# Optimization experiments

Measured on AMD Instinct MI355X. Metric: run time of the kernel, lower is better.

The kernel has to match this reference:

```python
import jax, jax.numpy as jnp
import numpy as np

V, E, H, B, S, C = 50000, 300, 512, 128, 80, 6
HH = 2 * H  # hidden_dim * num_directions (BiDi=True)


def _gru_dir(x, w_ih, w_hh, b_ih, b_hh, reverse):
    # x: (b, t, e) -> (b, t, h); torch nn.GRU cell math
    Bv, T, _ = x.shape
    Hd = w_hh.shape[1]
    xg = jnp.einsum('bte,ge->btg', x, w_ih) + b_ih  # (b, t, 3h)
    if reverse:
        xg = xg[:, ::-1]
    def step(h, xt):
        gi_r, gi_z, gi_n = jnp.split(xt, 3, axis=-1)
        gh_r, gh_z, gh_n = jnp.split(h @ w_hh.T + b_hh, 3, axis=-1)
        r = jax.nn.sigmoid(gi_r + gh_r)
        z = jax.nn.sigmoid(gi_z + gh_z)
        n = jnp.tanh(gi_n + r * gh_n)
        hn = (1.0 - z) * n + z * h
        return hn, hn
    h0 = jnp.zeros((Bv, Hd), x.dtype)
    _, hs = jax.lax.scan(step, h0, jnp.swapaxes(xg, 0, 1))
    hs = jnp.swapaxes(hs, 0, 1)
    if reverse:
        hs = hs[:, ::-1]
    return hs


def _bigru(x, pf, pb):
    return jnp.concatenate([_gru_dir(x, *pf, reverse=False), _gru_dir(x, *pb, reverse=True)], axis=-1)


def _conv1d(x, w, b, d):
    y = jax.lax.conv_general_dilated(x, w, (1,), 'VALID', rhs_dilation=(d,),
                                     dimension_numbers=('NCH', 'OIH', 'NCH'))
    return y + b[None, :, None]


def _bn(x, g, b, m, v):
    # eval-mode BatchNorm1d with running stats
    return (x - m[None, :, None]) * (g[None, :, None] / jnp.sqrt(v[None, :, None] + 1e-5)) + b[None, :, None]


def setup_inputs():
    key = jax.random.key(0)
    ks = iter(jax.random.split(key, 64))
    def W(*shape):
        return jax.random.normal(next(ks), shape, jnp.float32) * 0.02
    inp = {
        'input_batch': jax.random.randint(next(ks), (B, S), 1, V),
        'choices_batch': jax.random.randint(next(ks), (B, 4, C), 1, V),
        'emb_table': W(V, E),
    }
    for p in ('sg', 'cg'):
        for d in ('f', 'b'):
            inp[p + '_wih_' + d] = W(3 * H, E)
            inp[p + '_whh_' + d] = W(3 * H, H)
            inp[p + '_bih_' + d] = W(3 * H)
            inp[p + '_bhh_' + d] = W(3 * H)
    inp['lin_w'] = W(HH, HH * C)
    inp['lin_b'] = W(HH)
    inp['attn_w'] = W(HH, HH)
    inp['attn_b'] = W(HH)
    inp['c11_w'] = W(HH, S, 3);  inp['c11_b'] = W(HH)
    inp['c13_w'] = W(HH, HH, 3); inp['c13_b'] = W(HH)
    inp['c21_w'] = W(HH, HH, 3); inp['c21_b'] = W(HH)
    inp['c23_w'] = W(HH, HH, 3); inp['c23_b'] = W(HH)
    for i in ('1', '2'):
        inp['bn' + i + '_g'] = jnp.ones((HH,), jnp.float32)
        inp['bn' + i + '_b'] = jnp.zeros((HH,), jnp.float32)
        inp['bn' + i + '_m'] = jnp.zeros((HH,), jnp.float32)
        inp['bn' + i + '_v'] = jnp.ones((HH,), jnp.float32)
    inp['gate_wp'] = W(2 * HH, HH)
    inp['gate_wc'] = W(2 * HH, 2 * HH)
    inp['gate_b'] = W(2 * HH)
    inp['out_wp'] = W(2 * HH, HH)
    inp['out_b'] = W(2 * HH)
    return inp


def reference(input_batch, choices_batch, emb_table,
              sg_wih_f, sg_whh_f, sg_bih_f, sg_bhh_f, sg_wih_b, sg_whh_b, sg_bih_b, sg_bhh_b,
              cg_wih_f, cg_whh_f, cg_bih_f, cg_bhh_f, cg_wih_b, cg_whh_b, cg_bih_b, cg_bhh_b,
              lin_w, lin_b, attn_w, attn_b,
              c11_w, c11_b, c13_w, c13_b, c21_w, c21_b, c23_w, c23_b,
              bn1_g, bn1_b, bn1_m, bn1_v, bn2_g, bn2_b, bn2_m, bn2_v,
              gate_wp, gate_wc, gate_b, out_wp, out_b):
    # --- encode passage: embedding + BiGRU (dropout is eval-mode identity) ---
    sent = _bigru(emb_table[input_batch],
                  (sg_wih_f, sg_whh_f, sg_bih_f, sg_bhh_f),
                  (sg_wih_b, sg_whh_b, sg_bih_b, sg_bhh_b))  # (B, S, 2h)
    cgf = (cg_wih_f, cg_whh_f, cg_bih_f, cg_bhh_f)
    cgb = (cg_wih_b, cg_whh_b, cg_bih_b, cg_bhh_b)

    def choice_vec(tok):  # (B, C) -> (B, 2h)
        g = _bigru(emb_table[tok], cgf, cgb)               # (B, C, 2h)
        return g.reshape(g.shape[0], -1) @ lin_w.T + lin_b

    cvs = [choice_vec(choices_batch[:, i]) for i in range(4)]

    # --- AttnReader: shared Wh/bh, per-choice softmax attention over seq ---
    Wh = jnp.einsum('bsh,hg->bsg', sent, attn_w)  # (B, S, 2h)
    bh = sent @ attn_b                            # (B, S)

    def attn_read(cv):
        a = jax.nn.softmax(jnp.einsum('bsg,bg->bs', Wh, cv) + bh, axis=1)
        return jnp.einsum('bs,bsh->bh', a, sent)  # (B, 2h)

    pars = [attn_read(cv) for cv in cvs]

    # --- IDCNN: Conv1d treats seq dim S as channels (faithful to source) ---
    x = jax.nn.relu(_bn(_conv1d(sent, c11_w, c11_b, 1), bn1_g, bn1_b, bn1_m, bn1_v))
    x = _conv1d(x, c13_w, c13_b, 3)
    x = jax.nn.relu(_bn(_conv1d(x, c21_w, c21_b, 1), bn2_g, bn2_b, bn2_m, bn2_v))
    x = _conv1d(x, c23_w, c23_b, 3)
    P = jnp.max(x, axis=2)  # AdaptiveMaxPool1d(1) + squeeze -> (B, 2h)

    Cs = [jnp.concatenate([cv, par], axis=1) for cv, par in zip(cvs, pars)]  # (B, 4h)

    # --- PointerNet (note: source bug makes out1..out4 all equal C1WP+bC1) ---
    WP = P @ gate_wp.T          # (B, 4h)
    WP_out = P @ out_wp.T       # (B, 4h)
    Cd1 = Cs[0] * jax.nn.sigmoid(WP + Cs[0] @ gate_wc.T + gate_b)
    o1 = jnp.sum(Cd1 * WP_out, axis=1, keepdims=True) + (Cd1 @ out_b)[:, None]  # (B, 1)
    return jnp.concatenate([o1, o1, o1, o1], axis=1)  # (B, 4)
```

## Files before the change

### kernel.cpp

```cpp
#include <hip/hip_runtime.h>

typedef unsigned int u32;
typedef unsigned short u16;
typedef __attribute__((ext_vector_type(4))) float f32x4;
typedef __attribute__((ext_vector_type(8))) short bf16x8;

#define DEV static __device__ __forceinline__

DEV float sigf(float x){ return 1.0f/(1.0f + expf(-x)); }

DEV u16 f2bf(float x){
  u32 u = __float_as_uint(x);
  u32 r = (u + 0x7FFFu + ((u >> 16) & 1u)) >> 16;
  return (u16)r;
}

DEV u32 encf(float f){
  u32 u = __float_as_uint(f);
  return (u & 0x80000000u) ? ~u : (u | 0x80000000u);
}
DEV float decf(u32 e){
  return (e & 0x80000000u) ? __uint_as_float(e ^ 0x80000000u) : __uint_as_float(~e);
}

DEV void gload16(const void* g, void* l){
  __builtin_amdgcn_global_load_lds((const __attribute__((address_space(1))) u32*)g,
                                   (__attribute__((address_space(3))) u32*)l, 16, 0, 0);
}

__global__ __launch_bounds__(256,2) void gemm_bf16(
    const u16* __restrict__ A, const u16* __restrict__ A2,
    const u16* __restrict__ B,
    const float* __restrict__ bias, const float* __restrict__ bias2,
    float* __restrict__ C, float* __restrict__ C2, int ldc,
    int Kp, int ksteps)
{
  __shared__ u16 lds[(128 + 128)*32];
  char* ldsc = (char*)&lds[0];
  const int Boff = 128*64;
  const int tid = threadIdx.x;
  const int l = tid & 63, w = tid >> 6;
  const int n0 = blockIdx.x * 128, m0 = blockIdx.y * 128;
  const u16* Ause = blockIdx.z ? A2 : A;
  const float* buse = blockIdx.z ? bias2 : bias;
  float* Cuse = blockIdx.z ? C2 : C;
  const int wr = w >> 1, wc = w & 1;
  const int lr = l & 15, g = l >> 4;

  f32x4 acc[4][4];
  #pragma unroll
  for (int i=0;i<4;++i)
    #pragma unroll
    for (int j=0;j<4;++j) acc[i][j] = f32x4{0.f,0.f,0.f,0.f};

  for (int ks = 0; ks < ksteps; ++ks) {
    const int i0 = ks*32;
    __syncthreads();
    #pragma unroll
    for (int r = 0; r < 2; ++r) {
      const int rr = w*2 + r;
      const int c = rr*64 + l;
      const int row = c >> 2, bpos = c & 3;
      const int ib = bpos ^ ((row>>1) & 3);
      gload16(Ause + ((size_t)(m0 + row)*Kp + (i0 + ib*8)), ldsc + rr*1024);
      gload16(B    + ((size_t)(n0 + row)*Kp + (i0 + ib*8)), ldsc + Boff + rr*1024);
    }
    __syncthreads();
    bf16x8 af[4], bfr[4];
    #pragma unroll
    for (int m=0;m<4;++m){
      int o = wr*64 + m*16 + lr;
      af[m] = *(const bf16x8*)(ldsc + o*64 + ((g ^ ((o>>1)&3))<<4));
    }
    #pragma unroll
    for (int n=0;n<4;++n){
      int pr = wc*64 + n*16 + lr;
      bfr[n] = *(const bf16x8*)(ldsc + Boff + pr*64 + ((g ^ ((pr>>1)&3))<<4));
    }
    #pragma unroll
    for (int m=0;m<4;++m)
      #pragma unroll
      for (int n=0;n<4;++n)
        acc[m][n] = __builtin_amdgcn_mfma_f32_16x16x32_bf16(af[m], bfr[n], acc[m][n], 0,0,0);
  }

  #pragma unroll
  for (int m=0;m<4;++m){
    int mm = m0 + wr*64 + m*16 + g*4;
    f32x4 bv = *(const f32x4*)(buse + mm);
    #pragma unroll
    for (int n=0;n<4;++n){
      int p = n0 + wc*64 + n*16 + lr;
      f32x4 v;
      #pragma unroll
      for (int r2=0;r2<4;++r2) v[r2] = acc[m][n][r2] + bv[r2];
      *(f32x4*)(Cuse + (size_t)p*ldc + mm) = v;
    }
  }
}

__global__ __launch_bounds__(256,2) void gemm_bf16_sk(
    const u16* __restrict__ A, const u16* __restrict__ B,
    float* __restrict__ C, int ldc, int Kp, int kpc)
{
  __shared__ u16 lds[(128 + 128)*32];
  char* ldsc = (char*)&lds[0];
  const int Boff = 128*64;
  const int tid = threadIdx.x;
  const int l = tid & 63, w = tid >> 6;
  const int n0 = blockIdx.x * 128, m0 = blockIdx.y * 128;
  const int ks0 = blockIdx.z * kpc;
  const int wr = w >> 1, wc = w & 1;
  const int lr = l & 15, g = l >> 4;

  f32x4 acc[4][4];
  #pragma unroll
  for (int i=0;i<4;++i)
    #pragma unroll
    for (int j=0;j<4;++j) acc[i][j] = f32x4{0.f,0.f,0.f,0.f};

  for (int ks = 0; ks < kpc; ++ks) {
    const int i0 = (ks0 + ks)*32;
    __syncthreads();
    #pragma unroll
    for (int r = 0; r < 2; ++r) {
      const int rr = w*2 + r;
      const int c = rr*64 + l;
      const int row = c >> 2, bpos = c & 3;
      const int ib = bpos ^ ((row>>1) & 3);
      gload16(A + ((size_t)(m0 + row)*Kp + (i0 + ib*8)), ldsc + rr*1024);
      gload16(B + ((size_t)(n0 + row)*Kp + (i0 + ib*8)), ldsc + Boff + rr*1024);
    }
    __syncthreads();
    bf16x8 af[4], bfr[4];
    #pragma unroll
    for (int m=0;m<4;++m){
      int o = wr*64 + m*16 + lr;
      af[m] = *(const bf16x8*)(ldsc + o*64 + ((g ^ ((o>>1)&3))<<4));
    }
    #pragma unroll
    for (int n=0;n<4;++n){
      int pr = wc*64 + n*16 + lr;
      bfr[n] = *(const bf16x8*)(ldsc + Boff + pr*64 + ((g ^ ((pr>>1)&3))<<4));
    }
    #pragma unroll
    for (int m=0;m<4;++m)
      #pragma unroll
      for (int n=0;n<4;++n)
        acc[m][n] = __builtin_amdgcn_mfma_f32_16x16x32_bf16(af[m], bfr[n], acc[m][n], 0,0,0);
  }

  #pragma unroll
  for (int m=0;m<4;++m){
    int mm = m0 + wr*64 + m*16 + g*4;
    #pragma unroll
    for (int n=0;n<4;++n){
      int p = n0 + wc*64 + n*16 + lr;
      float* dst = C + (size_t)p*ldc + mm;
      #pragma unroll
      for (int r2=0;r2<4;++r2) atomicAdd(dst + r2, acc[m][n][r2]);
    }
  }
}

__global__ void initc(float* __restrict__ C, const float* __restrict__ bias,
                      int total, int mmask)
{
  int i = blockIdx.x*256 + threadIdx.x;
  if (i < total) C[i] = bias ? bias[i & mmask] : 0.f;
}

__global__ __launch_bounds__(256) void gru_step(
    const float* __restrict__ xg0, const float* __restrict__ xg1,
    const float* __restrict__ whh0, const float* __restrict__ whh1,
    const float* __restrict__ bhh0, const float* __restrict__ bhh1,
    float* __restrict__ hs, int S, int t)
{
  __shared__ float hL[32*520];
  __shared__ float wL[48*132];
  const int tid = threadIdx.x;
  const int tj = tid & 15, tb = tid >> 4;
  const int jg = blockIdx.x;
  const int b0 = blockIdx.y*32;
  const int dir = blockIdx.z;
  const int l = tid & 63, w = tid >> 6;
  const float* xg  = dir ? xg1  : xg0;
  const float* whh = dir ? whh1 : whh0;
  const float* bhh = dir ? bhh1 : bhh0;
  const int tt = dir ? (S-1-t) : t;
  const int j = jg*16 + tj;

  float accr[2], accz[2], accn[2];
  {
    float br = bhh[j], bz = bhh[512+j], bn = bhh[1024+j];
    accr[0]=br; accr[1]=br; accz[0]=bz; accz[1]=bz; accn[0]=bn; accn[1]=bn;
  }

  if (t > 0){
    const int tp = dir ? (tt+1) : (tt-1);
    #pragma unroll
    for (int rr = 0; rr < 8; ++rr){
      int row = w*8 + rr;
      const float* srcb = hs + ((size_t)(b0+row)*S + tp)*1024 + dir*512;
      gload16(srcb + l*4,       (char*)hL + (size_t)(row*520)*4);
      gload16(srcb + 256 + l*4, (char*)hL + (size_t)(row*520 + 256)*4);
    }
    for (int c = 0; c < 4; ++c){
      const int k0 = c*128;
      __syncthreads();
      #pragma unroll
      for (int i = 0; i < 6; ++i){
        int qidx = tid + i*256;
        int row = qidx >> 5, q = qidx & 31;
        int grow = (row>>4)*512 + jg*16 + (row & 15);
        f32x4 v = *(const f32x4*)(whh + (size_t)grow*512 + k0 + q*4);
        *(f32x4*)(wL + row*132 + q*4) = v;
      }
      __syncthreads();
      #pragma unroll 4
      for (int q = 0; q < 32; ++q){
        f32x4 ha  = *(const f32x4*)(hL + (2*tb  )*520 + k0 + q*4);
        f32x4 hb  = *(const f32x4*)(hL + (2*tb+1)*520 + k0 + q*4);
        f32x4 wr4 = *(const f32x4*)(wL + tj*132      + q*4);
        f32x4 wz4 = *(const f32x4*)(wL + (16+tj)*132 + q*4);
        f32x4 wn4 = *(const f32x4*)(wL + (32+tj)*132 + q*4);
        #pragma unroll
        for (int e = 0; e < 4; ++e){
          accr[0] += ha[e]*wr4[e]; accz[0] += ha[e]*wz4[e]; accn[0] += ha[e]*wn4[e];
          accr[1] += hb[e]*wr4[e]; accz[1] += hb[e]*wz4[e]; accn[1] += hb[e]*wn4[e];
        }
      }
    }
  }

  #pragma unroll
  for (int bi = 0; bi < 2; ++bi){
    int lb = 2*tb + bi;
    int b = b0 + lb;
    size_t xbase = ((size_t)b*S + tt)*1536;
    float gir = xg[xbase + j], giz = xg[xbase + 512 + j], gin = xg[xbase + 1024 + j];
    float hp = (t>0) ? hL[lb*520 + j] : 0.f;
    float r = sigf(gir + accr[bi]);
    float z = sigf(giz + accz[bi]);
    float n = tanhf(gin + r*accn[bi]);
    hs[((size_t)b*S + tt)*1024 + dir*512 + j] = (1.f - z)*n + z*hp;
  }
}

__global__ void transpose_sent(const float* __restrict__ sent, u16* __restrict__ sentT)
{
  __shared__ float tl[80][65];
  int b = blockIdx.y, h0 = blockIdx.x*64;
  for (int idx = threadIdx.x; idx < 80*64; idx += 256){
    int s = idx >> 6, hh = idx & 63;
    tl[s][hh] = sent[((size_t)b*80 + s)*1024 + h0 + hh];
  }
  __syncthreads();
  for (int idx = threadIdx.x; idx < 64*96; idx += 256){
    int hh = idx / 96, s = idx % 96;
    sentT[((size_t)b*1024 + h0 + hh)*96 + s] = (s < 80) ? f2bf(tl[s][hh]) : (u16)0;
  }
}

__global__ void attn_scores(const float* __restrict__ sent, const float* __restrict__ u,
                            const float* __restrict__ attn_b, float* __restrict__ sc)
{
  int wid = blockIdx.x*4 + (threadIdx.x >> 6);
  int lane = threadIdx.x & 63;
  const float* row = sent + (size_t)wid*1024;
  const float* ub = u + (size_t)(wid/80)*1024;
  float acc = 0.f;
  for (int h = lane; h < 1024; h += 64) acc += row[h]*(ub[h] + attn_b[h]);
  #pragma unroll
  for (int m = 32; m; m >>= 1) acc += __shfl_xor(acc, m);
  if (lane == 0) sc[wid] = acc;
}

__global__ void softmax80(const float* __restrict__ sc, float* __restrict__ a)
{
  int b = blockIdx.x, l = threadIdx.x;
  float v0 = sc[b*80 + l];
  float v1 = (l < 16) ? sc[b*80 + 64 + l] : -1e30f;
  float mx = fmaxf(v0, v1);
  #pragma unroll
  for (int m = 32; m; m >>= 1) mx = fmaxf(mx, __shfl_xor(mx, m));
  float e0 = expf(v0 - mx);
  float e1 = (l < 16) ? expf(v1 - mx) : 0.f;
  float s = e0 + e1;
  #pragma unroll
  for (int m = 32; m; m >>= 1) s += __shfl_xor(s, m);
  float inv = 1.f/s;
  a[b*80 + l] = e0*inv;
  if (l < 16) a[b*80 + 64 + l] = e1*inv;
}

__global__ void par_cs0(const float* __restrict__ a, const float* __restrict__ sent,
                        const float* __restrict__ cv, float* __restrict__ Cs0)
{
  int b = blockIdx.x;
  for (int h = threadIdx.x; h < 1024; h += 256){
    float acc = 0.f;
    for (int s = 0; s < 80; ++s) acc += a[b*80+s]*sent[((size_t)b*80+s)*1024 + h];
    Cs0[(size_t)b*2048 + 1024 + h] = acc;
    Cs0[(size_t)b*2048 + h] = cv[(size_t)b*1024 + h];
  }
}

__global__ void pack_w(const float* __restrict__ src, u16* __restrict__ dst,
                       int O, int CIs, int CIp)
{
  int i = blockIdx.x*256 + threadIdx.x;
  int total = 3*O*CIp;
  if (i >= total) return;
  int tap = i/(O*CIp); int rem = i%(O*CIp); int o = rem/CIp, ci = rem%CIp;
  float v = (ci < CIs) ? src[((size_t)o*CIs + ci)*3 + tap] : 0.f;
  dst[((size_t)tap*O + o)*CIp + ci] = f2bf(v);
}

__global__ void pack_wk(const float* __restrict__ src, u16* __restrict__ dst,
                        int M, int Ks, int Kp)
{
  int i = blockIdx.x*256 + threadIdx.x;
  if (i >= M*Kp) return;
  int row = i/Kp, k = i%Kp;
  dst[i] = (k < Ks) ? f2bf(src[(size_t)row*Ks + k]) : (u16)0;
}

__global__ void pack_f2b(const float* __restrict__ src, u16* __restrict__ dst, int n)
{
  int i = blockIdx.x*256 + threadIdx.x;
  if (i < n) dst[i] = f2bf(src[i]);
}

__global__ void pack_x(const float* __restrict__ emb, const int* __restrict__ toks,
                       int rdiv, int rmul, u16* __restrict__ dst, int R)
{
  int i = blockIdx.x*256 + threadIdx.x;
  if (i >= R*320) return;
  int row = i/320, k = i%320;
  int tok = toks[(row/rdiv)*rmul + (row%rdiv)];
  dst[i] = (k < 300) ? f2bf(emb[(size_t)tok*300 + k]) : (u16)0;
}

__global__ void prep_ab(const float* c11b, const float* c13b, const float* c21b, const float* c23b,
                        const float* g1, const float* b1, const float* m1, const float* v1,
                        const float* g2, const float* b2, const float* m2, const float* v2,
                        float* ab)
{
  int i = blockIdx.x*256 + threadIdx.x;
  if (i >= 4096) return;
  int layer = i >> 10, o = i & 1023;
  float al, be;
  if (layer == 0){ al = g1[o]/sqrtf(v1[o]+1e-5f); be = c11b[o]*al + b1[o] - m1[o]*al; }
  else if (layer == 1){ al = 1.f; be = c13b[o]; }
  else if (layer == 2){ al = g2[o]/sqrtf(v2[o]+1e-5f); be = c21b[o]*al + b2[o] - m2[o]*al; }
  else { al = 1.f; be = c23b[o]; }
  ab[layer*2048 + o] = al;
  ab[layer*2048 + 1024 + o] = be;
}

__global__ void init_penc(u32* p){
  int i = blockIdx.x*256 + threadIdx.x;
  if (i < 128*1024) p[i] = encf(-3.3e38f);
}
__global__ void dec_p(const u32* __restrict__ pe, float* __restrict__ pf){
  int i = blockIdx.x*256 + threadIdx.x;
  if (i < 128*1024) pf[i] = decf(pe[i]);
}

__global__ __launch_bounds__(512,2) void conv_mfma(
    const u16* __restrict__ X, long bstrideX,
    const u16* __restrict__ Wt,
    const float* __restrict__ alpha, const float* __restrict__ beta,
    u16* __restrict__ Y, long bstrideY,
    u32* __restrict__ Penc, int b0,
    int P_in, int P_out, int CI, int dil, int ksteps, int mode)
{
  __shared__ u16 lds[2*66560/2];
  char* ldsc = (char*)&lds[0];
  const int BUF = 66560;
  const int BOFF = 768*64;
  const int tid = threadIdx.x;
  const int l = tid & 63, w = tid >> 6;
  const int wg = blockIdx.x + (blockIdx.y<<2) + (blockIdx.z<<4);
  const int id2 = ((wg & 7) << 5) | (wg >> 3);
  const int p0 = (id2 & 3) * 256;
  const int o0 = ((id2 >> 2) & 3) * 256;
  const int bz = id2 >> 4;
  const u16* Xb = X + (size_t)bz * (size_t)bstrideX;
  const int wr = w >> 2, wc = w & 3;
  const int lr = l & 15, g = l >> 4;

  f32x4 acc[8][4];
  #pragma unroll
  for (int i=0;i<8;++i)
    #pragma unroll
    for (int j=0;j<4;++j) acc[i][j] = f32x4{0.f,0.f,0.f,0.f};

  {
    const int i0 = 0;
    #pragma unroll
    for (int r = 0; r < 6; ++r) {
      const int c = r*512 + tid;
      const int row = c >> 2, bpos = c & 3;
      const int tap = row >> 8, o = row & 255;
      const int ib = bpos ^ ((row>>1) & 3);
      gload16(Wt + ((size_t)(tap*1024 + o0 + o)*CI + (i0 + ib*8)), ldsc + (size_t)c*16);
    }
    #pragma unroll
    for (int r = 0; r < 3; ++r) {
      const int c = r*512 + tid;
      if (c < 1088){
        const int row = c >> 2, bpos = c & 3;
        const int ib = bpos ^ ((row>>1) & 3);
        int ps = p0 + row; ps = ps < P_in ? ps : (P_in - 1);
        gload16(Xb + ((size_t)ps*CI + (i0 + ib*8)), ldsc + BOFF + (size_t)c*16);
      }
    }
  }
  __syncthreads();

  for (int ks = 0; ks < ksteps; ++ks) {
    const int cur = ks & 1;
    if (ks + 1 < ksteps) {
      const int i0 = (ks+1)*32;
      char* dst = ldsc + (cur^1)*BUF;
      #pragma unroll
      for (int r = 0; r < 6; ++r) {
        const int c = r*512 + tid;
        const int row = c >> 2, bpos = c & 3;
        const int tap = row >> 8, o = row & 255;
        const int ib = bpos ^ ((row>>1) & 3);
        gload16(Wt + ((size_t)(tap*1024 + o0 + o)*CI + (i0 + ib*8)), dst + (size_t)c*16);
      }
      #pragma unroll
      for (int r = 0; r < 3; ++r) {
        const int c = r*512 + tid;
        if (c < 1088){
          const int row = c >> 2, bpos = c & 3;
          const int ib = bpos ^ ((row>>1) & 3);
          int ps = p0 + row; ps = ps < P_in ? ps : (P_in - 1);
          gload16(Xb + ((size_t)ps*CI + (i0 + ib*8)), dst + BOFF + (size_t)c*16);
        }
      }
    }
    char* src = ldsc + cur*BUF;
    #pragma unroll
    for (int tap = 0; tap < 3; ++tap) {
      bf16x8 af[8];
      #pragma unroll
      for (int m=0;m<8;++m){
        int o = wr*128 + m*16 + lr;
        int row = tap*256 + o;
        af[m] = *(const bf16x8*)(src + row*64 + ((g ^ ((row>>1)&3))<<4));
      }
      #pragma unroll
      for (int n=0;n<4;++n){
        int pr = wc*64 + n*16 + lr + dil*tap;
        bf16x8 bfr = *(const bf16x8*)(src + BOFF + pr*64 + ((g ^ ((pr>>1)&3))<<4));
        #pragma unroll
        for (int m=0;m<8;++m)
          acc[m][n] = __builtin_amdgcn_mfma_f32_16x16x32_bf16(af[m], bfr, acc[m][n], 0,0,0);
      }
    }
    __syncthreads();
  }

  if (mode == 2) {
    #pragma unroll
    for (int m=0;m<8;++m){
      int oo = o0 + wr*128 + m*16 + g*4;
      f32x4 al = *(const f32x4*)(alpha + oo);
      f32x4 be = *(const f32x4*)(beta + oo);
      float vm[4] = {-1e30f,-1e30f,-1e30f,-1e30f};
      #pragma unroll
      for (int n=0;n<4;++n){
        int p = p0 + wc*64 + n*16 + lr;
        bool ok = p < P_out;
        #pragma unroll
        for (int r2=0;r2<4;++r2){
          float v = acc[m][n][r2]*al[r2] + be[r2];
          vm[r2] = ok ? fmaxf(vm[r2], v) : vm[r2];
        }
      }
      #pragma unroll
      for (int r2=0;r2<4;++r2){
        float v = vm[r2];
        #pragma unroll
        for (int mask=1; mask<16; mask<<=1) v = fmaxf(v, __shfl_xor(v, mask));
        if (lr == 0) atomicMax(&Penc[(size_t)(b0+bz)*1024 + oo + r2], encf(v));
      }
    }
  } else {
    #pragma unroll
    for (int m=0;m<8;++m){
      int oo = o0 + wr*128 + m*16 + g*4;
      f32x4 al = *(const f32x4*)(alpha + oo);
      f32x4 be = *(const f32x4*)(beta + oo);
      #pragma unroll
      for (int n=0;n<4;++n){
        int p = p0 + wc*64 + n*16 + lr;
        if (p < P_out){
          float v0 = acc[m][n][0]*al[0] + be[0];
          float v1 = acc[m][n][1]*al[1] + be[1];
          float v2 = acc[m][n][2]*al[2] + be[2];
          float v3 = acc[m][n][3]*al[3] + be[3];
          if (mode == 0){ v0=fmaxf(v0,0.f); v1=fmaxf(v1,0.f); v2=fmaxf(v2,0.f); v3=fmaxf(v3,0.f); }
          uint2 pk;
          pk.x = (u32)f2bf(v0) | ((u32)f2bf(v1) << 16);
          pk.y = (u32)f2bf(v2) | ((u32)f2bf(v3) << 16);
          *(uint2*)(Y + (size_t)bz*(size_t)bstrideY + (size_t)p*1024 + oo) = pk;
        }
      }
    }
  }
}

__global__ void head_final(const float* __restrict__ Cs0, const float* __restrict__ t1,
                           const float* __restrict__ t2, const float* __restrict__ outb,
                           float* __restrict__ dout)
{
  __shared__ float red[256];
  int b = blockIdx.x;
  float part = 0.f;
  for (int gg = threadIdx.x; gg < 2048; gg += 256){
    float cd = Cs0[(size_t)b*2048+gg] * sigf(t1[(size_t)b*2048+gg]);
    part += cd * (t2[(size_t)b*2048+gg] + outb[gg]);
  }
  red[threadIdx.x] = part;
  __syncthreads();
  for (int s = 128; s > 0; s >>= 1){
    if (threadIdx.x < s) red[threadIdx.x] += red[threadIdx.x + s];
    __syncthreads();
  }
  if (threadIdx.x < 4) dout[b*4 + threadIdx.x] = red[0];
}

extern "C" void kernel_launch(void* const* d_in, const int* in_sizes, int n_in,
                              void* d_out, int out_size, void* d_ws, size_t ws_size,
                              hipStream_t stream)
{
  (void)in_sizes; (void)n_in; (void)out_size; (void)ws_size;
  const int*   input_batch = (const int*)d_in[0];
  const int*   choices     = (const int*)d_in[1];
  const float* emb    = (const float*)d_in[2];
  const float* sgwihf = (const float*)d_in[3];
  const float* sgwhhf = (const float*)d_in[4];
  const float* sgbihf = (const float*)d_in[5];
  const float* sgbhhf = (const float*)d_in[6];
  const float* sgwihb = (const float*)d_in[7];
  const float* sgwhhb = (const float*)d_in[8];
  const float* sgbihb = (const float*)d_in[9];
  const float* sgbhhb = (const float*)d_in[10];
  const float* cgwihf = (const float*)d_in[11];
  const float* cgwhhf = (const float*)d_in[12];
  const float* cgbihf = (const float*)d_in[13];
  const float* cgbhhf = (const float*)d_in[14];
  const float* cgwihb = (const float*)d_in[15];
  const float* cgwhhb = (const float*)d_in[16];
  const float* cgbihb = (const float*)d_in[17];
  const float* cgbhhb = (const float*)d_in[18];
  const float* lin_w  = (const float*)d_in[19];
  const float* lin_b  = (const float*)d_in[20];
  const float* attn_w = (const float*)d_in[21];
  const float* attn_b = (const float*)d_in[22];
  const float* c11w = (const float*)d_in[23];
  const float* c11b = (const float*)d_in[24];
  const float* c13w = (const float*)d_in[25];
  const float* c13b = (const float*)d_in[26];
  const float* c21w = (const float*)d_in[27];
  const float* c21b = (const float*)d_in[28];
  const float* c23w = (const float*)d_in[29];
  const float* c23b = (const float*)d_in[30];
  const float* bn1g = (const float*)d_in[31];
  const float* bn1b = (const float*)d_in[32];
  const float* bn1m = (const float*)d_in[33];
  const float* bn1v = (const float*)d_in[34];
  const float* bn2g = (const float*)d_in[35];
  const float* bn2b = (const float*)d_in[36];
  const float* bn2m = (const float*)d_in[37];
  const float* bn2v = (const float*)d_in[38];
  const float* gatewp = (const float*)d_in[39];
  const float* gatewc = (const float*)d_in[40];
  const float* gateb  = (const float*)d_in[41];
  const float* outwp  = (const float*)d_in[42];
  const float* outb   = (const float*)d_in[43];
  float* dout = (float*)d_out;

  char* ws = (char*)d_ws; size_t off = 0;
  auto alc = [&](size_t n)->char*{ char* p = ws + off; off = (off + n + 255) & ~(size_t)255; return p; };
  float* xg_f  = (float*)alc((size_t)128*80*1536*4);
  float* xg_b  = (float*)alc((size_t)128*80*1536*4);
  float* xg_cf = (float*)alc((size_t)128*6*1536*4);
  float* xg_cb = (float*)alc((size_t)128*6*1536*4);
  float* gh    = (float*)alc((size_t)2*128*1536*4); (void)gh;
  float* sent  = (float*)alc((size_t)128*80*1024*4);
  float* g_c   = (float*)alc((size_t)128*6*1024*4);
  u16*   sentT = (u16*)alc((size_t)128*1024*96*2);
  float* cv    = (float*)alc((size_t)128*1024*4);
  float* uu    = (float*)alc((size_t)128*1024*4);
  float* scb   = (float*)alc((size_t)128*80*4);
  float* aw    = (float*)alc((size_t)128*80*4);
  float* Cs0   = (float*)alc((size_t)128*2048*4);
  u16* W1p = (u16*)alc((size_t)3*1024*96*2);
  u16* W2p = (u16*)alc((size_t)3*1024*1024*2);
  u16* W3p = (u16*)alc((size_t)3*1024*1024*2);
  u16* W4p = (u16*)alc((size_t)3*1024*1024*2);
  float* ab  = (float*)alc((size_t)4*2048*4);
  u32*  Penc = (u32*)alc((size_t)128*1024*4);
  float* Pf  = (float*)alc((size_t)128*1024*4);
  float* t1  = (float*)alc((size_t)128*2048*4);
  float* t2  = (float*)alc((size_t)128*2048*4);
  u16* xbf_s = (u16*)alc((size_t)10240*320*2);
  u16* xbf_c = (u16*)alc((size_t)768*320*2);
  u16* Wsf = (u16*)alc((size_t)1536*320*2);
  u16* Wsb = (u16*)alc((size_t)1536*320*2);
  u16* Wcf = (u16*)alc((size_t)1536*320*2);
  u16* Wcb = (u16*)alc((size_t)1536*320*2);

  char* R1 = (char*)xg_f;
  u16* linw_bf  = (u16*)(R1);
  u16* attnw_bf = (u16*)(R1 + 12582912);
  u16* gcbf     = (u16*)(R1 + 14680064);
  u16* cvbf     = (u16*)(R1 + 16252928);
  const int bc = 16;
  u16* Y0 = (u16*)(R1 + 16515072);
  u16* Y1 = Y0 + (size_t)bc*1024*1024;
  char* R2 = (char*)sent;
  u16* gwp_bf = (u16*)(R2);
  u16* gwc_bf = (u16*)(R2 + 4194304);
  u16* owp_bf = (u16*)(R2 + 12582912);
  u16* Pfbf   = (u16*)(R2 + 16777216);
  u16* Cs0bf  = (u16*)(R2 + 17039360);

  dim3 T(256), T5(512);

  pack_w<<<dim3((3*1024*96+255)/256), T, 0, stream>>>(c11w, W1p, 1024, 80, 96);
  pack_w<<<dim3((3*1024*1024+255)/256), T, 0, stream>>>(c13w, W2p, 1024, 1024, 1024);
  pack_w<<<dim3((3*1024*1024+255)/256), T, 0, stream>>>(c21w, W3p, 1024, 1024, 1024);
  pack_w<<<dim3((3*1024*1024+255)/256), T, 0, stream>>>(c23w, W4p, 1024, 1024, 1024);
  pack_wk<<<dim3((1536*320+255)/256), T, 0, stream>>>(sgwihf, Wsf, 1536, 300, 320);
  pack_wk<<<dim3((1536*320+255)/256), T, 0, stream>>>(sgwihb, Wsb, 1536, 300, 320);
  pack_wk<<<dim3((1536*320+255)/256), T, 0, stream>>>(cgwihf, Wcf, 1536, 300, 320);
  pack_wk<<<dim3((1536*320+255)/256), T, 0, stream>>>(cgwihb, Wcb, 1536, 300, 320);
  pack_x<<<dim3((10240*320+255)/256), T, 0, stream>>>(emb, input_batch, 80, 80, xbf_s, 10240);
  pack_x<<<dim3((768*320+255)/256), T, 0, stream>>>(emb, choices, 6, 24, xbf_c, 768);
  prep_ab<<<16, T, 0, stream>>>(c11b, c13b, c21b, c23b,
                                bn1g,bn1b,bn1m,bn1v, bn2g,bn2b,bn2m,bn2v, ab);
  init_penc<<<512, T, 0, stream>>>(Penc);

  gemm_bf16<<<dim3(80,12,2), T, 0, stream>>>(Wsf, Wsb, xbf_s, sgbihf, sgbihb,
                                             xg_f, xg_b, 1536, 320, 10);
  gemm_bf16<<<dim3(6,12,2), T, 0, stream>>>(Wcf, Wcb, xbf_c, cgbihf, cgbihb,
                                            xg_cf, xg_cb, 1536, 320, 10);

  for (int t = 0; t < 80; ++t)
    gru_step<<<dim3(32,4,2), T, 0, stream>>>(xg_f, xg_b, sgwhhf, sgwhhb,
                                             sgbhhf, sgbhhb, sent, 80, t);
  for (int t = 0; t < 6; ++t)
    gru_step<<<dim3(32,4,2), T, 0, stream>>>(xg_cf, xg_cb, cgwhhf, cgwhhb,
                                             cgbhhf, cgbhhb, g_c, 6, t);

  pack_wk<<<dim3((1024*6144+255)/256), T, 0, stream>>>(lin_w, linw_bf, 1024, 6144, 6144);
  pack_wk<<<dim3((1024*1024+255)/256), T, 0, stream>>>(attn_w, attnw_bf, 1024, 1024, 1024);
  pack_f2b<<<dim3((128*6144+255)/256), T, 0, stream>>>(g_c, gcbf, 128*6144);

  transpose_sent<<<dim3(16,128), T, 0, stream>>>(sent, sentT);

  initc<<<dim3((128*1024+255)/256), T, 0, stream>>>(cv, lin_b, 128*1024, 1023);
  gemm_bf16_sk<<<dim3(1,8,6), T, 0, stream>>>(linw_bf, gcbf, cv, 1024, 6144, 32);
  pack_f2b<<<dim3((128*1024+255)/256), T, 0, stream>>>(cv, cvbf, 128*1024);
  initc<<<dim3((128*1024+255)/256), T, 0, stream>>>(uu, nullptr, 128*1024, 1023);
  gemm_bf16_sk<<<dim3(1,8,2), T, 0, stream>>>(attnw_bf, cvbf, uu, 1024, 1024, 16);
  attn_scores<<<2560, T, 0, stream>>>(sent, uu, attn_b, scb);
  softmax80<<<128, dim3(64), 0, stream>>>(scb, aw);
  par_cs0<<<128, T, 0, stream>>>(aw, sent, cv, Cs0);

  pack_wk<<<dim3((2048*1024+255)/256), T, 0, stream>>>(gatewp, gwp_bf, 2048, 1024, 1024);
  pack_wk<<<dim3((2048*2048+255)/256), T, 0, stream>>>(gatewc, gwc_bf, 2048, 2048, 2048);
  pack_wk<<<dim3((2048*1024+255)/256), T, 0, stream>>>(outwp, owp_bf, 2048, 1024, 1024);
  pack_f2b<<<dim3((128*2048+255)/256), T, 0, stream>>>(Cs0, Cs0bf, 128*2048);

  for (int b0 = 0; b0 < 128; b0 += bc){
    conv_mfma<<<dim3(4,4,bc), T5, 0, stream>>>(sentT + (size_t)b0*1024*96, (long)1024*96,
        W1p, ab+0,    ab+1024, Y0, (long)1024*1024, nullptr, 0, 1024, 1022, 96,   1, 3,  0);
    conv_mfma<<<dim3(4,4,bc), T5, 0, stream>>>(Y0, (long)1024*1024,
        W2p, ab+2048, ab+3072, Y1, (long)1024*1024, nullptr, 0, 1022, 1016, 1024, 3, 32, 1);
    conv_mfma<<<dim3(4,4,bc), T5, 0, stream>>>(Y1, (long)1024*1024,
        W3p, ab+4096, ab+5120, Y0, (long)1024*1024, nullptr, 0, 1016, 1014, 1024, 1, 32, 0);
    conv_mfma<<<dim3(4,4,bc), T5, 0, stream>>>(Y0, (long)1024*1024,
        W4p, ab+6144, ab+7168, nullptr, 0, Penc, b0,          1014, 1008, 1024, 3, 32, 2);
  }
  dec_p<<<512, T, 0, stream>>>(Penc, Pf);
  pack_f2b<<<dim3((128*1024+255)/256), T, 0, stream>>>(Pf, Pfbf, 128*1024);

  initc<<<dim3((128*2048+255)/256), T, 0, stream>>>(t1, gateb, 128*2048, 2047);
  gemm_bf16_sk<<<dim3(1,16,2), T, 0, stream>>>(gwp_bf, Pfbf, t1, 2048, 1024, 16);
  gemm_bf16_sk<<<dim3(1,16,4), T, 0, stream>>>(gwc_bf, Cs0bf, t1, 2048, 2048, 16);
  initc<<<dim3((128*2048+255)/256), T, 0, stream>>>(t2, nullptr, 128*2048, 2047);
  gemm_bf16_sk<<<dim3(1,16,2), T, 0, stream>>>(owp_bf, Pfbf, t2, 2048, 1024, 16);
  head_final<<<128, T, 0, stream>>>(Cs0, t1, t2, outb, dout);
}
```

Measured before the change: 3.720 ms.

## Overlap conv prefetch loads with MFMA compute using per-wave vmcnt waits

```diff
diff --git a/kernel.cpp b/kernel.cpp
--- a/kernel.cpp
+++ b/kernel.cpp
@@ -368,6 +368,36 @@
   if (i < 128*1024) pf[i] = decf(pe[i]);
 }
 
+#define CONV_STAGE(DST, I0)                                                   \
+  {                                                                           \
+    _Pragma("unroll")                                                         \
+    for (int r = 0; r < 6; ++r) {                                             \
+      const int c = r*512 + tid;                                              \
+      const int row = c >> 2, bpos = c & 3;                                   \
+      const int tap = row >> 8, o = row & 255;                                \
+      const int ib = bpos ^ ((row>>1) & 3);                                   \
+      gload16(Wt + ((size_t)(tap*1024 + o0 + o)*CI + ((I0) + ib*8)),          \
+              (DST) + (size_t)c*16);                                          \
+    }                                                                         \
+    _Pragma("unroll")                                                         \
+    for (int r = 0; r < 2; ++r) {                                             \
+      const int c = w*136 + r*64 + l;                                         \
+      const int row = c >> 2, bpos = c & 3;                                   \
+      const int ib = bpos ^ ((row>>1) & 3);                                   \
+      int ps = p0 + row; ps = ps < P_in ? ps : (P_in - 1);                    \
+      gload16(Xb + ((size_t)ps*CI + ((I0) + ib*8)),                           \
+              (DST) + BOFF + (size_t)c*16);                                   \
+    }                                                                         \
+    if (l < 8) {                                                              \
+      const int c = w*136 + 128 + l;                                          \
+      const int row = c >> 2, bpos = c & 3;                                   \
+      const int ib = bpos ^ ((row>>1) & 3);                                   \
+      int ps = p0 + row; ps = ps < P_in ? ps : (P_in - 1);                    \
+      gload16(Xb + ((size_t)ps*CI + ((I0) + ib*8)),                           \
+              (DST) + BOFF + (size_t)c*16);                                   \
+    }                                                                         \
+  }
+
 __global__ __launch_bounds__(512,2) void conv_mfma(
     const u16* __restrict__ X, long bstrideX,
     const u16* __restrict__ Wt,
@@ -376,7 +406,7 @@
     u32* __restrict__ Penc, int b0,
     int P_in, int P_out, int CI, int dil, int ksteps, int mode)
 {
-  __shared__ u16 lds[2*66560/2];
+  __shared__ u16 lds[66560];
   char* ldsc = (char*)&lds[0];
   const int BUF = 66560;
   const int BOFF = 768*64;
@@ -397,54 +427,22 @@
     #pragma unroll
     for (int j=0;j<4;++j) acc[i][j] = f32x4{0.f,0.f,0.f,0.f};
 
-  {
-    const int i0 = 0;
-    #pragma unroll
-    for (int r = 0; r < 6; ++r) {
-      const int c = r*512 + tid;
-      const int row = c >> 2, bpos = c & 3;
-      const int tap = row >> 8, o = row & 255;
-      const int ib = bpos ^ ((row>>1) & 3);
-      gload16(Wt + ((size_t)(tap*1024 + o0 + o)*CI + (i0 + ib*8)), ldsc + (size_t)c*16);
-    }
-    #pragma unroll
-    for (int r = 0; r < 3; ++r) {
-      const int c = r*512 + tid;
-      if (c < 1088){
-        const int row = c >> 2, bpos = c & 3;
-        const int ib = bpos ^ ((row>>1) & 3);
-        int ps = p0 + row; ps = ps < P_in ? ps : (P_in - 1);
-        gload16(Xb + ((size_t)ps*CI + (i0 + ib*8)), ldsc + BOFF + (size_t)c*16);
-      }
-    }
-  }
-  __syncthreads();
+  CONV_STAGE(ldsc, 0)
 
   for (int ks = 0; ks < ksteps; ++ks) {
     const int cur = ks & 1;
     if (ks + 1 < ksteps) {
-      const int i0 = (ks+1)*32;
       char* dst = ldsc + (cur^1)*BUF;
-      #pragma unroll
-      for (int r = 0; r < 6; ++r) {
-        const int c = r*512 + tid;
-        const int row = c >> 2, bpos = c & 3;
-        const int tap = row >> 8, o = row & 255;
-        const int ib = bpos ^ ((row>>1) & 3);
-        gload16(Wt + ((size_t)(tap*1024 + o0 + o)*CI + (i0 + ib*8)), dst + (size_t)c*16);
-      }
-      #pragma unroll
-      for (int r = 0; r < 3; ++r) {
-        const int c = r*512 + tid;
-        if (c < 1088){
-          const int row = c >> 2, bpos = c & 3;
-          const int ib = bpos ^ ((row>>1) & 3);
-          int ps = p0 + row; ps = ps < P_in ? ps : (P_in - 1);
-          gload16(Xb + ((size_t)ps*CI + (i0 + ib*8)), dst + BOFF + (size_t)c*16);
-        }
-      }
-    }
+      CONV_STAGE(dst, (ks+1)*32)
+      asm volatile("s_waitcnt vmcnt(9)" ::: "memory");
+    } else {
+      asm volatile("s_waitcnt vmcnt(0)" ::: "memory");
+    }
+    __builtin_amdgcn_s_barrier();
+    asm volatile("" ::: "memory");
+
     char* src = ldsc + cur*BUF;
+    __builtin_amdgcn_s_setprio(1);
     #pragma unroll
     for (int tap = 0; tap < 3; ++tap) {
       bf16x8 af[8];
@@ -463,7 +461,11 @@
           acc[m][n] = __builtin_amdgcn_mfma_f32_16x16x32_bf16(af[m], bfr, acc[m][n], 0,0,0);
       }
     }
-    __syncthreads();
+    __builtin_amdgcn_s_setprio(0);
+
+    asm volatile("s_waitcnt lgkmcnt(0)" ::: "memory");
+    __builtin_amdgcn_s_barrier();
+    asm volatile("" ::: "memory");
   }
 
   if (mode == 2) {
```

Measured after the change: 3.981 ms. 7.0% more time.

## Pipeline conv MFMA per tap with 4-slot LDS ring and fine-grained waits

Applied to the files above, without the earlier changes.

```diff
diff --git a/kernel.cpp b/kernel.cpp
--- a/kernel.cpp
+++ b/kernel.cpp
@@ -368,6 +368,67 @@
   if (i < 128*1024) pf[i] = decf(pe[i]);
 }
 
+#define CPHASE(KS, TAP, NSTR)                                                 \
+  {                                                                           \
+    char* Aslot = ldsc + ((((KS)*3 + (TAP)) & 3) << 14);                      \
+    char* Bbuf  = ldsc + 65536 + (((KS)&1) ? 17408 : 0);                      \
+    bf16x8 af[8], bfr[4];                                                     \
+    _Pragma("unroll")                                                         \
+    for (int m=0;m<8;++m){                                                    \
+      int o = wr*128 + m*16 + lr;                                             \
+      af[m] = *(const bf16x8*)(Aslot + o*64 + ((g ^ ((o>>1)&3))<<4));         \
+    }                                                                         \
+    _Pragma("unroll")                                                         \
+    for (int n=0;n<4;++n){                                                    \
+      int pr = wc*64 + n*16 + lr + dil*(TAP);                                 \
+      bfr[n] = *(const bf16x8*)(Bbuf + pr*64 + ((g ^ ((pr>>1)&3))<<4));       \
+    }                                                                         \
+    if ((KS)+1 < ksteps) {                                                    \
+      char* Adst = ldsc + ((((KS)*3 + (TAP) + 3) & 3) << 14);                 \
+      const int i0n = ((KS)+1)*32;                                            \
+      _Pragma("unroll")                                                       \
+      for (int r = 0; r < 2; ++r) {                                           \
+        const int c = r*512 + tid;                                            \
+        const int row = c >> 2, bpos = c & 3;                                 \
+        const int ib = bpos ^ ((row>>1) & 3);                                 \
+        gload16(Wt + ((size_t)((TAP)*1024 + o0 + row)*CI + (i0n + ib*8)),     \
+                Adst + (size_t)c*16);                                         \
+      }                                                                       \
+      if ((TAP) == 0) {                                                       \
+        char* Bdst = ldsc + 65536 + ((((KS)+1)&1) ? 17408 : 0);               \
+        _Pragma("unroll")                                                     \
+        for (int r = 0; r < 2; ++r) {                                         \
+          const int c = w*136 + r*64 + l;                                     \
+          const int row = c >> 2, bpos = c & 3;                               \
+          const int ib = bpos ^ ((row>>1) & 3);                               \
+          int ps = p0 + row; ps = ps < P_in ? ps : (P_in - 1);                \
+          gload16(Xb + ((size_t)ps*CI + (i0n + ib*8)), Bdst + (size_t)c*16);  \
+        }                                                                     \
+        if (l < 8) {                                                          \
+          const int c = w*136 + 128 + l;                                      \
+          const int row = c >> 2, bpos = c & 3;                               \
+          const int ib = bpos ^ ((row>>1) & 3);                               \
+          int ps = p0 + row; ps = ps < P_in ? ps : (P_in - 1);                \
+          gload16(Xb + ((size_t)ps*CI + (i0n + ib*8)), Bdst + (size_t)c*16);  \
+        }                                                                     \
+      }                                                                       \
+    }                                                                         \
+    asm volatile("s_waitcnt vmcnt(" NSTR ")" ::: "memory");                   \
+    __builtin_amdgcn_s_barrier();                                             \
+    asm volatile("" ::: "memory");                                            \
+    __builtin_amdgcn_s_setprio(1);                                            \
+    _Pragma("unroll")                                                         \
+    for (int n=0;n<4;++n)                                                     \
+      _Pragma("unroll")                                                       \
+      for (int m=0;m<8;++m)                                                   \
+        acc[m][n] = __builtin_amdgcn_mfma_f32_16x16x32_bf16(af[m], bfr[n],    \
+                                                            acc[m][n], 0,0,0);\
+    __builtin_amdgcn_s_setprio(0);                                            \
+    asm volatile("" ::: "memory");                                            \
+    __builtin_amdgcn_s_barrier();                                             \
+    asm volatile("" ::: "memory");                                            \
+  }
+
 __global__ __launch_bounds__(512,2) void conv_mfma(
     const u16* __restrict__ X, long bstrideX,
     const u16* __restrict__ Wt,
@@ -376,10 +437,8 @@
     u32* __restrict__ Penc, int b0,
     int P_in, int P_out, int CI, int dil, int ksteps, int mode)
 {
-  __shared__ u16 lds[2*66560/2];
+  __shared__ u16 lds[50176];
   char* ldsc = (char*)&lds[0];
-  const int BUF = 66560;
-  const int BOFF = 768*64;
   const int tid = threadIdx.x;
   const int l = tid & 63, w = tid >> 6;
   const int wg = blockIdx.x + (blockIdx.y<<2) + (blockIdx.z<<4);
@@ -397,73 +456,49 @@
     #pragma unroll
     for (int j=0;j<4;++j) acc[i][j] = f32x4{0.f,0.f,0.f,0.f};
 
-  {
-    const int i0 = 0;
-    #pragma unroll
-    for (int r = 0; r < 6; ++r) {
+  #pragma unroll
+  for (int t = 0; t < 3; ++t){
+    char* Adst = ldsc + (t << 14);
+    #pragma unroll
+    for (int r = 0; r < 2; ++r) {
       const int c = r*512 + tid;
       const int row = c >> 2, bpos = c & 3;
-      const int tap = row >> 8, o = row & 255;
       const int ib = bpos ^ ((row>>1) & 3);
-      gload16(Wt + ((size_t)(tap*1024 + o0 + o)*CI + (i0 + ib*8)), ldsc + (size_t)c*16);
-    }
-    #pragma unroll
-    for (int r = 0; r < 3; ++r) {
-      const int c = r*512 + tid;
-      if (c < 1088){
-        const int row = c >> 2, bpos = c & 3;
-        const int ib = bpos ^ ((row>>1) & 3);
-        int ps = p0 + row; ps = ps < P_in ? ps : (P_in - 1);
-        gload16(Xb + ((size_t)ps*CI + (i0 + ib*8)), ldsc + BOFF + (size_t)c*16);
-      }
-    }
-  }
-  __syncthreads();
-
-  for (int ks = 0; ks < ksteps; ++ks) {
-    const int cur = ks & 1;
-    if (ks + 1 < ksteps) {
-      const int i0 = (ks+1)*32;
-      char* dst = ldsc + (cur^1)*BUF;
-      #pragma unroll
-      for (int r = 0; r < 6; ++r) {
-        const int c = r*512 + tid;
-        const int row = c >> 2, bpos = c & 3;
-        const int tap = row >> 8, o = row & 255;
-        const int ib = bpos ^ ((row>>1) & 3);
-        gload16(Wt + ((size_t)(tap*1024 + o0 + o)*CI + (i0 + ib*8)), dst + (size_t)c*16);
-      }
-      #pragma unroll
-      for (int r = 0; r < 3; ++r) {
-        const int c = r*512 + tid;
-        if (c < 1088){
-          const int row = c >> 2, bpos = c & 3;
-          const int ib = bpos ^ ((row>>1) & 3);
-          int ps = p0 + row; ps = ps < P_in ? ps : (P_in - 1);
-          gload16(Xb + ((size_t)ps*CI + (i0 + ib*8)), dst + BOFF + (size_t)c*16);
-        }
-      }
-    }
-    char* src = ldsc + cur*BUF;
-    #pragma unroll
-    for (int tap = 0; tap < 3; ++tap) {
-      bf16x8 af[8];
-      #pragma unroll
-      for (int m=0;m<8;++m){
-        int o = wr*128 + m*16 + lr;
-        int row = tap*256 + o;
-        af[m] = *(const bf16x8*)(src + row*64 + ((g ^ ((row>>1)&3))<<4));
-      }
-      #pragma unroll
-      for (int n=0;n<4;++n){
-        int pr = wc*64 + n*16 + lr + dil*tap;
-        bf16x8 bfr = *(const bf16x8*)(src + BOFF + pr*64 + ((g ^ ((pr>>1)&3))<<4));
-        #pragma unroll
-        for (int m=0;m<8;++m)
-          acc[m][n] = __builtin_amdgcn_mfma_f32_16x16x32_bf16(af[m], bfr, acc[m][n], 0,0,0);
-      }
-    }
-    __syncthreads();
+      gload16(Wt + ((size_t)(t*1024 + o0 + row)*CI + (ib*8)), Adst + (size_t)c*16);
+    }
+  }
+  {
+    char* Bdst = ldsc + 65536;
+    #pragma unroll
+    for (int r = 0; r < 2; ++r) {
+      const int c = w*136 + r*64 + l;
+      const int row = c >> 2, bpos = c & 3;
+      const int ib = bpos ^ ((row>>1) & 3);
+      int ps = p0 + row; ps = ps < P_in ? ps : (P_in - 1);
+      gload16(Xb + ((size_t)ps*CI + (ib*8)), Bdst + (size_t)c*16);
+    }
+    if (l < 8) {
+      const int c = w*136 + 128 + l;
+      const int row = c >> 2, bpos = c & 3;
+      const int ib = bpos ^ ((row>>1) & 3);
+      int ps = p0 + row; ps = ps < P_in ? ps : (P_in - 1);
+      gload16(Xb + ((size_t)ps*CI + (ib*8)), Bdst + (size_t)c*16);
+    }
+  }
+  asm volatile("s_waitcnt vmcnt(0)" ::: "memory");
+  __builtin_amdgcn_s_barrier();
+  asm volatile("" ::: "memory");
+
+  for (int ks = 0; ks < ksteps-1; ++ks) {
+    CPHASE(ks, 0, "7")
+    CPHASE(ks, 1, "7")
+    CPHASE(ks, 2, "4")
+  }
+  {
+    const int ks = ksteps-1;
+    CPHASE(ks, 0, "0")
+    CPHASE(ks, 1, "0")
+    CPHASE(ks, 2, "0")
   }
 
   if (mode == 2) {
```

Result: slower. 3.864 ms (+3.9%).
